# Optimization experiments

Measured on AMD Instinct MI355X. Metric: run time of the kernel, lower is better.

The kernel has to match this reference:

```python
import jax, jax.numpy as jnp
import numpy as np

N_NODES = 100000
N_EDGES = 1600000
HIDDEN = 128
N_STRUCT = 6
N_LAYERS = 3
BN_EPS = 1e-5


def setup_inputs() -> dict:
    key = jax.random.key(0)
    ks = jax.random.split(key, 8)
    edge_index = jax.random.randint(ks[0], (2, N_EDGES), 0, N_NODES, dtype=jnp.int32)
    struct_feats = jax.random.uniform(ks[1], (N_NODES, N_STRUCT), dtype=jnp.float32)
    emb_weight = jax.random.normal(ks[2], (N_NODES, HIDDEN - N_STRUCT), dtype=jnp.float32) * 0.1
    proj_w = jax.random.normal(ks[3], (N_STRUCT, N_STRUCT), dtype=jnp.float32) * 0.4
    proj_b = jnp.zeros((N_STRUCT,), jnp.float32)
    conv_w = jax.random.normal(ks[4], (N_LAYERS, HIDDEN, HIDDEN), dtype=jnp.float32) * (1.0 / np.sqrt(HIDDEN))
    conv_b = jnp.zeros((N_LAYERS, HIDDEN), jnp.float32)
    bn_gamma = jnp.ones((N_LAYERS, HIDDEN), jnp.float32)
    bn_beta = jnp.zeros((N_LAYERS, HIDDEN), jnp.float32)
    bn_mean = jnp.zeros((N_LAYERS, HIDDEN), jnp.float32)
    bn_var = jnp.ones((N_LAYERS, HIDDEN), jnp.float32)
    return {
        'edge_index': edge_index, 'struct_feats': struct_feats,
        'emb_weight': emb_weight, 'proj_w': proj_w, 'proj_b': proj_b,
        'conv_w': conv_w, 'conv_b': conv_b,
        'bn_gamma': bn_gamma, 'bn_beta': bn_beta,
        'bn_mean': bn_mean, 'bn_var': bn_var,
    }


def _encode(edge_index, struct_feats, emb_weight, proj_w, proj_b,
            conv_w, conv_b, bn_gamma, bn_beta, bn_mean, bn_var):
    src, dst = edge_index[0], edge_index[1]
    # GCN symmetric normalization (no self loops): deg over destination index
    deg = jax.ops.segment_sum(jnp.ones_like(src, dtype=jnp.float32), dst,
                              num_segments=N_NODES)
    dinv = jnp.where(deg > 0, jax.lax.rsqrt(deg), 0.0)
    norm = dinv[src] * dinv[dst]  # [E]

    # node features: learned embedding || projected structural features
    sf = jax.nn.relu(struct_feats @ proj_w + proj_b)
    x = jnp.concatenate([emb_weight, sf], axis=1)  # [N, HIDDEN]

    for i in range(N_LAYERS):
        x_prev = x
        h = x @ conv_w[i]  # [N, H]
        msg = h[src] * norm[:, None]  # gather + scale, [E, H]
        agg = jax.ops.segment_sum(msg, dst, num_segments=N_NODES) + conv_b[i]
        # BatchNorm1d (eval mode, running stats)
        x = (agg - bn_mean[i]) * (bn_gamma[i] * jax.lax.rsqrt(bn_var[i] + BN_EPS)) + bn_beta[i]
        x = jax.nn.relu(x)
        if i > 0:
            x = x + 0.5 * x_prev
    return x


def reference(edge_index, struct_feats, emb_weight, proj_w, proj_b,
              conv_w, conv_b, bn_gamma, bn_beta, bn_mean, bn_var):
    return _encode(edge_index, struct_feats, emb_weight, proj_w, proj_b,
                   conv_w, conv_b, bn_gamma, bn_beta, bn_mean, bn_var)
```

## Files before the change

### kernel.cpp

```cpp
#include <hip/hip_runtime.h>
#include <hip/hip_fp16.h>

#define N_NODES 100000
#define N_EDGES 1600000
#define HIDDEN  128
#define EMB_DIM 122
#define NSTRUCT 6
#define BN_EPS  1e-5f

__global__ void k_count_deg(const int* __restrict__ dst, int* __restrict__ deg,
                            int* __restrict__ rank) {
    int i = blockIdx.x * blockDim.x + threadIdx.x;
    if (i < N_EDGES) rank[i] = atomicAdd(&deg[dst[i]], 1);
}

#define SCAN_B 256
__global__ void k_scan1(const int* __restrict__ deg, int* __restrict__ bsum) {
    __shared__ int s[SCAN_B];
    int t = threadIdx.x;
    int i = blockIdx.x * SCAN_B + t;
    s[t] = (i < N_NODES) ? deg[i] : 0;
    __syncthreads();
    for (int off = SCAN_B / 2; off > 0; off >>= 1) {
        if (t < off) s[t] += s[t + off];
        __syncthreads();
    }
    if (t == 0) bsum[blockIdx.x] = s[0];
}

__global__ void k_scan2(int* __restrict__ bsum, int nb, int* __restrict__ ptrN) {
    __shared__ int s[512];
    int t = threadIdx.x;
    int v = (t < nb) ? bsum[t] : 0;
    s[t] = v;
    __syncthreads();
    for (int off = 1; off < 512; off <<= 1) {
        int u = (t >= off) ? s[t - off] : 0;
        __syncthreads();
        s[t] += u;
        __syncthreads();
    }
    if (t < nb) bsum[t] = s[t] - v;
    if (t == nb - 1) *ptrN = s[t];
}

__global__ void k_scan3(const int* __restrict__ deg, const int* __restrict__ bsum,
                        int* __restrict__ ptr) {
    __shared__ int s[SCAN_B];
    int t = threadIdx.x;
    int i = blockIdx.x * SCAN_B + t;
    int v = (i < N_NODES) ? deg[i] : 0;
    s[t] = v;
    __syncthreads();
    for (int off = 1; off < SCAN_B; off <<= 1) {
        int u = (t >= off) ? s[t - off] : 0;
        __syncthreads();
        s[t] += u;
        __syncthreads();
    }
    if (i < N_NODES) ptr[i] = bsum[blockIdx.x] + s[t] - v;
}

__global__ void k_fill(const int* __restrict__ src, const int* __restrict__ dst,
                       const int* __restrict__ rank,
                       const int* __restrict__ deg, const int* __restrict__ ptr,
                       int2* __restrict__ edges) {
    int i = blockIdx.x * blockDim.x + threadIdx.x;
    if (i < N_EDGES) {
        int s = src[i], d = dst[i];
        int ds = deg[s], dd = deg[d];
        float ns = (ds > 0) ? rsqrtf((float)ds) : 0.0f;
        float nd = (dd > 0) ? rsqrtf((float)dd) : 0.0f;
        int pos = ptr[d] + rank[i];
        edges[pos] = make_int2(s, __float_as_int(ns * nd));
    }
}

__global__ void k_node_init(const float* __restrict__ emb, const float* __restrict__ sfeat,
                            const float* __restrict__ pw, const float* __restrict__ pb,
                            float* __restrict__ x) {
    int idx = blockIdx.x * blockDim.x + threadIdx.x;
    if (idx >= N_NODES * HIDDEN) return;
    int n = idx >> 7, c = idx & 127;
    float v;
    if (c < EMB_DIM) {
        v = emb[n * EMB_DIM + c];
    } else {
        int j = c - EMB_DIM;
        float a = pb[j];
        #pragma unroll
        for (int k = 0; k < NSTRUCT; ++k) a += sfeat[n * NSTRUCT + k] * pw[k * NSTRUCT + j];
        v = fmaxf(a, 0.0f);
    }
    x[idx] = v;
}

__global__ __launch_bounds__(256, 3)
void k_gemm(const float* __restrict__ x, const float* __restrict__ W,
            __half* __restrict__ h) {
    __shared__ float Ws[64 * HIDDEN];
    __shared__ float xs[64][65];

    const int tid = threadIdx.x;
    const int n0  = blockIdx.x * 64;
    const int cg  = tid & 15;
    const int rg  = tid >> 4;
    const int c0  = cg * 4;
    const int r0  = rg * 4;

    float acc[4][8];
    #pragma unroll
    for (int i = 0; i < 4; ++i)
        #pragma unroll
        for (int j = 0; j < 8; ++j) acc[i][j] = 0.0f;

    for (int kk = 0; kk < HIDDEN; kk += 64) {
        for (int i = tid; i < 64 * HIDDEN; i += 256) Ws[i] = W[kk * HIDDEN + i];
        for (int i = tid; i < 64 * 64; i += 256) {
            int r = i >> 6, k = i & 63;
            int gn = n0 + r;
            xs[r][k] = (gn < N_NODES) ? x[(size_t)gn * HIDDEN + kk + k] : 0.0f;
        }
        __syncthreads();

        #pragma unroll 4
        for (int k = 0; k < 64; ++k) {
            float4 wa = *reinterpret_cast<const float4*>(&Ws[k * HIDDEN + c0]);
            float4 wb = *reinterpret_cast<const float4*>(&Ws[k * HIDDEN + c0 + 64]);
            #pragma unroll
            for (int i = 0; i < 4; ++i) {
                float xv = xs[r0 + i][k];
                acc[i][0] = fmaf(xv, wa.x, acc[i][0]);
                acc[i][1] = fmaf(xv, wa.y, acc[i][1]);
                acc[i][2] = fmaf(xv, wa.z, acc[i][2]);
                acc[i][3] = fmaf(xv, wa.w, acc[i][3]);
                acc[i][4] = fmaf(xv, wb.x, acc[i][4]);
                acc[i][5] = fmaf(xv, wb.y, acc[i][5]);
                acc[i][6] = fmaf(xv, wb.z, acc[i][6]);
                acc[i][7] = fmaf(xv, wb.w, acc[i][7]);
            }
        }
        __syncthreads();
    }

    #pragma unroll
    for (int i = 0; i < 4; ++i) {
        int gn = n0 + r0 + i;
        if (gn < N_NODES) {
            union { uint2 u; __half2 h2[2]; } p0, p1;
            p0.h2[0] = __floats2half2_rn(acc[i][0], acc[i][1]);
            p0.h2[1] = __floats2half2_rn(acc[i][2], acc[i][3]);
            p1.h2[0] = __floats2half2_rn(acc[i][4], acc[i][5]);
            p1.h2[1] = __floats2half2_rn(acc[i][6], acc[i][7]);
            *reinterpret_cast<uint2*>(&h[(size_t)gn * HIDDEN + c0])      = p0.u;
            *reinterpret_cast<uint2*>(&h[(size_t)gn * HIDDEN + c0 + 64]) = p1.u;
        }
    }
}

__global__ __launch_bounds__(256)
void k_agg(const __half* __restrict__ h, const int* __restrict__ ptr,
           const int2* __restrict__ edges,
           const float* __restrict__ bias, const float* __restrict__ mean,
           const float* __restrict__ var, const float* __restrict__ gamma,
           const float* __restrict__ beta,
           const float* __restrict__ xprev, int has_resid,
           float* __restrict__ out) {
    int node = blockIdx.x * 4 + (threadIdx.x >> 6);
    if (node >= N_NODES) return;
    const int lane = threadIdx.x & 63;
    const int q    = lane >> 4;
    const int sl   = lane & 15;
    const int c0   = sl * 8;
    int s = ptr[node], e = ptr[node + 1];

    float acc[8];
    #pragma unroll
    for (int k = 0; k < 8; ++k) acc[k] = 0.0f;

    for (int j0 = s; j0 < e; j0 += 64) {
        int nb  = min(64, e - j0);
        int idx = j0 + lane;
        int2 rec = (idx < e) ? edges[idx] : make_int2(0, 0);
        #pragma unroll 2
        for (int jj = 0; jj < nb; jj += 4) {
            int   sv = __shfl(rec.x, jj + q);
            float nv = __int_as_float(__shfl(rec.y, jj + q));
            union { uint4 u; __half2 h2[4]; } v;
            v.u = *reinterpret_cast<const uint4*>(h + ((size_t)sv << 7) + c0);
            #pragma unroll
            for (int k = 0; k < 4; ++k) {
                float2 f = __half22float2(v.h2[k]);
                acc[2 * k]     = fmaf(nv, f.x, acc[2 * k]);
                acc[2 * k + 1] = fmaf(nv, f.y, acc[2 * k + 1]);
            }
        }
    }

    #pragma unroll
    for (int k = 0; k < 8; ++k) {
        acc[k] += __shfl_xor(acc[k], 16);
        acc[k] += __shfl_xor(acc[k], 32);
    }

    if (q == 0) {
        float4 bi0 = *reinterpret_cast<const float4*>(bias  + c0);
        float4 bi1 = *reinterpret_cast<const float4*>(bias  + c0 + 4);
        float4 mu0 = *reinterpret_cast<const float4*>(mean  + c0);
        float4 mu1 = *reinterpret_cast<const float4*>(mean  + c0 + 4);
        float4 va0 = *reinterpret_cast<const float4*>(var   + c0);
        float4 va1 = *reinterpret_cast<const float4*>(var   + c0 + 4);
        float4 ga0 = *reinterpret_cast<const float4*>(gamma + c0);
        float4 ga1 = *reinterpret_cast<const float4*>(gamma + c0 + 4);
        float4 be0 = *reinterpret_cast<const float4*>(beta  + c0);
        float4 be1 = *reinterpret_cast<const float4*>(beta  + c0 + 4);
        float4 y0, y1;
        y0.x = fmaxf((acc[0] + bi0.x - mu0.x) * (ga0.x * rsqrtf(va0.x + BN_EPS)) + be0.x, 0.0f);
        y0.y = fmaxf((acc[1] + bi0.y - mu0.y) * (ga0.y * rsqrtf(va0.y + BN_EPS)) + be0.y, 0.0f);
        y0.z = fmaxf((acc[2] + bi0.z - mu0.z) * (ga0.z * rsqrtf(va0.z + BN_EPS)) + be0.z, 0.0f);
        y0.w = fmaxf((acc[3] + bi0.w - mu0.w) * (ga0.w * rsqrtf(va0.w + BN_EPS)) + be0.w, 0.0f);
        y1.x = fmaxf((acc[4] + bi1.x - mu1.x) * (ga1.x * rsqrtf(va1.x + BN_EPS)) + be1.x, 0.0f);
        y1.y = fmaxf((acc[5] + bi1.y - mu1.y) * (ga1.y * rsqrtf(va1.y + BN_EPS)) + be1.y, 0.0f);
        y1.z = fmaxf((acc[6] + bi1.z - mu1.z) * (ga1.z * rsqrtf(va1.z + BN_EPS)) + be1.z, 0.0f);
        y1.w = fmaxf((acc[7] + bi1.w - mu1.w) * (ga1.w * rsqrtf(va1.w + BN_EPS)) + be1.w, 0.0f);
        size_t o = ((size_t)node << 7) + c0;
        if (has_resid) {
            float4 xp0 = *reinterpret_cast<const float4*>(xprev + o);
            float4 xp1 = *reinterpret_cast<const float4*>(xprev + o + 4);
            y0.x += 0.5f * xp0.x;  y0.y += 0.5f * xp0.y;
            y0.z += 0.5f * xp0.z;  y0.w += 0.5f * xp0.w;
            y1.x += 0.5f * xp1.x;  y1.y += 0.5f * xp1.y;
            y1.z += 0.5f * xp1.z;  y1.w += 0.5f * xp1.w;
        }
        *reinterpret_cast<float4*>(out + o)     = y0;
        *reinterpret_cast<float4*>(out + o + 4) = y1;
    }
}

extern "C" void kernel_launch(void* const* d_in, const int* in_sizes, int n_in,
                              void* d_out, int out_size, void* d_ws, size_t ws_size,
                              hipStream_t stream) {
    const int*   ei    = (const int*)d_in[0];
    const int*   src   = ei;
    const int*   dst   = ei + N_EDGES;
    const float* sfeat = (const float*)d_in[1];
    const float* emb   = (const float*)d_in[2];
    const float* pw    = (const float*)d_in[3];
    const float* pb    = (const float*)d_in[4];
    const float* convw = (const float*)d_in[5];
    const float* convb = (const float*)d_in[6];
    const float* gamma = (const float*)d_in[7];
    const float* beta  = (const float*)d_in[8];
    const float* mean  = (const float*)d_in[9];
    const float* var   = (const float*)d_in[10];
    float* out = (float*)d_out;

    char* wsc = (char*)d_ws;
    auto alloc = [&](size_t bytes) -> void* {
        void* p = (void*)wsc;
        wsc += (bytes + 255) & ~(size_t)255;
        return p;
    };
    int*    deg   = (int*)   alloc(N_NODES * sizeof(int));
    int*    rank  = (int*)   alloc((size_t)N_EDGES * sizeof(int));
    int*    ptr   = (int*)   alloc((N_NODES + 1) * sizeof(int));
    int*    bsum  = (int*)   alloc(512 * sizeof(int));
    int2*   edges = (int2*)  alloc((size_t)N_EDGES * sizeof(int2));
    float*  bufA  = (float*) alloc((size_t)N_NODES * HIDDEN * sizeof(float));
    __half* hbuf  = (__half*)alloc((size_t)N_NODES * HIDDEN * sizeof(__half));

    const int nb = (N_NODES + SCAN_B - 1) / SCAN_B;

    hipMemsetAsync(deg, 0, N_NODES * sizeof(int), stream);

    k_count_deg<<<N_EDGES / 256, 256, 0, stream>>>(dst, deg, rank);
    k_scan1<<<nb, SCAN_B, 0, stream>>>(deg, bsum);
    k_scan2<<<1, 512, 0, stream>>>(bsum, nb, &ptr[N_NODES]);
    k_scan3<<<nb, SCAN_B, 0, stream>>>(deg, bsum, ptr);
    k_fill<<<N_EDGES / 256, 256, 0, stream>>>(src, dst, rank, deg, ptr, edges);
    k_node_init<<<(N_NODES * HIDDEN) / 256, 256, 0, stream>>>(emb, sfeat, pw, pb, bufA);

    const int ggrid = (N_NODES + 63) / 64;
    const int agrid = (N_NODES + 3) / 4;

    k_gemm<<<ggrid, 256, 0, stream>>>(bufA, convw + 0 * HIDDEN * HIDDEN, hbuf);
    k_agg<<<agrid, 256, 0, stream>>>(hbuf, ptr, edges,
                                     convb + 0 * HIDDEN, mean + 0 * HIDDEN, var + 0 * HIDDEN,
                                     gamma + 0 * HIDDEN, beta + 0 * HIDDEN,
                                     nullptr, 0, bufA);
    k_gemm<<<ggrid, 256, 0, stream>>>(bufA, convw + 1 * HIDDEN * HIDDEN, hbuf);
    k_agg<<<agrid, 256, 0, stream>>>(hbuf, ptr, edges,
                                     convb + 1 * HIDDEN, mean + 1 * HIDDEN, var + 1 * HIDDEN,
                                     gamma + 1 * HIDDEN, beta + 1 * HIDDEN,
                                     bufA, 1, out);
    k_gemm<<<ggrid, 256, 0, stream>>>(out, convw + 2 * HIDDEN * HIDDEN, hbuf);
    k_agg<<<agrid, 256, 0, stream>>>(hbuf, ptr, edges,
                                     convb + 2 * HIDDEN, mean + 2 * HIDDEN, var + 2 * HIDDEN,
                                     gamma + 2 * HIDDEN, beta + 2 * HIDDEN,
                                     out, 1, out);
    (void)in_sizes; (void)n_in; (void)out_size; (void)ws_size;
}
```

Baseline: 667.1 us.

## Use fp16 MFMA for per-layer GEMM with pre-transposed half weights

Replaces the FP32 shared-memory tiled GEMM with a wave-level MFMA 16x16x32 f16 kernel. Activations are converted to fp16 in registers and weights are read from a transposed fp16 copy, which a new small kernel produces once per call. The aim is to cut the compute cost of the dense transform. In exchange, GEMM inputs now carry fp16 rounding, and the output stores are scattered 2-byte writes rather than vectorized ones.

```diff
diff --git a/kernel.cpp b/kernel.cpp
--- a/kernel.cpp
+++ b/kernel.cpp
@@ -7,6 +7,9 @@
 #define EMB_DIM 122
 #define NSTRUCT 6
 #define BN_EPS  1e-5f
+
+typedef _Float16 f16x8 __attribute__((ext_vector_type(8)));
+typedef float    f32x4 __attribute__((ext_vector_type(4)));
 
 __global__ void k_count_deg(const int* __restrict__ dst, int* __restrict__ deg,
                             int* __restrict__ rank) {
@@ -95,65 +98,59 @@
     x[idx] = v;
 }
 
-__global__ __launch_bounds__(256, 3)
-void k_gemm(const float* __restrict__ x, const float* __restrict__ W,
+__global__ void k_wcvt(const float* __restrict__ W, __half* __restrict__ Wt) {
+    int idx = blockIdx.x * blockDim.x + threadIdx.x;
+    int l = idx >> 14, rem = idx & 16383, n = rem >> 7, k = rem & 127;
+    Wt[idx] = __float2half(W[l * 16384 + k * 128 + n]);
+}
+
+__global__ __launch_bounds__(256)
+void k_gemm(const float* __restrict__ x, const __half* __restrict__ Wt,
             __half* __restrict__ h) {
-    __shared__ float Ws[64 * HIDDEN];
-    __shared__ float xs[64][65];
-
-    const int tid = threadIdx.x;
-    const int n0  = blockIdx.x * 64;
-    const int cg  = tid & 15;
-    const int rg  = tid >> 4;
-    const int c0  = cg * 4;
-    const int r0  = rg * 4;
-
-    float acc[4][8];
-    #pragma unroll
-    for (int i = 0; i < 4; ++i)
+    const int tid  = threadIdx.x;
+    const int w    = tid >> 6;
+    const int lane = tid & 63;
+    const int g    = lane >> 4;
+    const int m15  = lane & 15;
+
+    const int rowA = blockIdx.x * 64 + w * 16 + m15;
+    const bool rok = (rowA < N_NODES);
+
+    f32x4 acc[8];
+    #pragma unroll
+    for (int nt = 0; nt < 8; ++nt) acc[nt] = (f32x4){0.f, 0.f, 0.f, 0.f};
+
+    #pragma unroll
+    for (int kc = 0; kc < 4; ++kc) {
+        const int k0 = kc * 32 + g * 8;
+        f16x8 a;
+        if (rok) {
+            const float4 p0 = *reinterpret_cast<const float4*>(x + (size_t)rowA * HIDDEN + k0);
+            const float4 p1 = *reinterpret_cast<const float4*>(x + (size_t)rowA * HIDDEN + k0 + 4);
+            a[0] = (_Float16)p0.x; a[1] = (_Float16)p0.y;
+            a[2] = (_Float16)p0.z; a[3] = (_Float16)p0.w;
+            a[4] = (_Float16)p1.x; a[5] = (_Float16)p1.y;
+            a[6] = (_Float16)p1.z; a[7] = (_Float16)p1.w;
+        } else {
+            a = (f16x8)(_Float16)0;
+        }
         #pragma unroll
-        for (int j = 0; j < 8; ++j) acc[i][j] = 0.0f;
-
-    for (int kk = 0; kk < HIDDEN; kk += 64) {
-        for (int i = tid; i < 64 * HIDDEN; i += 256) Ws[i] = W[kk * HIDDEN + i];
-        for (int i = tid; i < 64 * 64; i += 256) {
-            int r = i >> 6, k = i & 63;
-            int gn = n0 + r;
-            xs[r][k] = (gn < N_NODES) ? x[(size_t)gn * HIDDEN + kk + k] : 0.0f;
-        }
-        __syncthreads();
-
-        #pragma unroll 4
-        for (int k = 0; k < 64; ++k) {
-            float4 wa = *reinterpret_cast<const float4*>(&Ws[k * HIDDEN + c0]);
-            float4 wb = *reinterpret_cast<const float4*>(&Ws[k * HIDDEN + c0 + 64]);
-            #pragma unroll
-            for (int i = 0; i < 4; ++i) {
-                float xv = xs[r0 + i][k];
-                acc[i][0] = fmaf(xv, wa.x, acc[i][0]);
-                acc[i][1] = fmaf(xv, wa.y, acc[i][1]);
-                acc[i][2] = fmaf(xv, wa.z, acc[i][2]);
-                acc[i][3] = fmaf(xv, wa.w, acc[i][3]);
-                acc[i][4] = fmaf(xv, wb.x, acc[i][4]);
-                acc[i][5] = fmaf(xv, wb.y, acc[i][5]);
-                acc[i][6] = fmaf(xv, wb.z, acc[i][6]);
-                acc[i][7] = fmaf(xv, wb.w, acc[i][7]);
-            }
-        }
-        __syncthreads();
-    }
-
-    #pragma unroll
-    for (int i = 0; i < 4; ++i) {
-        int gn = n0 + r0 + i;
-        if (gn < N_NODES) {
-            union { uint2 u; __half2 h2[2]; } p0, p1;
-            p0.h2[0] = __floats2half2_rn(acc[i][0], acc[i][1]);
-            p0.h2[1] = __floats2half2_rn(acc[i][2], acc[i][3]);
-            p1.h2[0] = __floats2half2_rn(acc[i][4], acc[i][5]);
-            p1.h2[1] = __floats2half2_rn(acc[i][6], acc[i][7]);
-            *reinterpret_cast<uint2*>(&h[(size_t)gn * HIDDEN + c0])      = p0.u;
-            *reinterpret_cast<uint2*>(&h[(size_t)gn * HIDDEN + c0 + 64]) = p1.u;
+        for (int nt = 0; nt < 8; ++nt) {
+            const int n = nt * 16 + m15;
+            f16x8 b = *reinterpret_cast<const f16x8*>(Wt + (size_t)n * HIDDEN + k0);
+            acc[nt] = __builtin_amdgcn_mfma_f32_16x16x32_f16(a, b, acc[nt], 0, 0, 0);
+        }
+    }
+
+    const int growbase = blockIdx.x * 64 + w * 16 + g * 4;
+    #pragma unroll
+    for (int nt = 0; nt < 8; ++nt) {
+        const int col = nt * 16 + m15;
+        #pragma unroll
+        for (int r = 0; r < 4; ++r) {
+            const int grow = growbase + r;
+            if (grow < N_NODES)
+                h[(size_t)grow * HIDDEN + col] = __float2half(acc[nt][r]);
         }
     }
 }
@@ -268,12 +265,14 @@
     int2*   edges = (int2*)  alloc((size_t)N_EDGES * sizeof(int2));
     float*  bufA  = (float*) alloc((size_t)N_NODES * HIDDEN * sizeof(float));
     __half* hbuf  = (__half*)alloc((size_t)N_NODES * HIDDEN * sizeof(__half));
+    __half* wt    = (__half*)alloc(3 * HIDDEN * HIDDEN * sizeof(__half));
 
     const int nb = (N_NODES + SCAN_B - 1) / SCAN_B;
 
     hipMemsetAsync(deg, 0, N_NODES * sizeof(int), stream);
 
     k_count_deg<<<N_EDGES / 256, 256, 0, stream>>>(dst, deg, rank);
+    k_wcvt<<<(3 * HIDDEN * HIDDEN) / 256, 256, 0, stream>>>(convw, wt);
     k_scan1<<<nb, SCAN_B, 0, stream>>>(deg, bsum);
     k_scan2<<<1, 512, 0, stream>>>(bsum, nb, &ptr[N_NODES]);
     k_scan3<<<nb, SCAN_B, 0, stream>>>(deg, bsum, ptr);
@@ -283,17 +282,17 @@
     const int ggrid = (N_NODES + 63) / 64;
     const int agrid = (N_NODES + 3) / 4;
 
-    k_gemm<<<ggrid, 256, 0, stream>>>(bufA, convw + 0 * HIDDEN * HIDDEN, hbuf);
+    k_gemm<<<ggrid, 256, 0, stream>>>(bufA, wt + 0 * HIDDEN * HIDDEN, hbuf);
     k_agg<<<agrid, 256, 0, stream>>>(hbuf, ptr, edges,
                                      convb + 0 * HIDDEN, mean + 0 * HIDDEN, var + 0 * HIDDEN,
                                      gamma + 0 * HIDDEN, beta + 0 * HIDDEN,
                                      nullptr, 0, bufA);
-    k_gemm<<<ggrid, 256, 0, stream>>>(bufA, convw + 1 * HIDDEN * HIDDEN, hbuf);
+    k_gemm<<<ggrid, 256, 0, stream>>>(bufA, wt + 1 * HIDDEN * HIDDEN, hbuf);
     k_agg<<<agrid, 256, 0, stream>>>(hbuf, ptr, edges,
                                      convb + 1 * HIDDEN, mean + 1 * HIDDEN, var + 1 * HIDDEN,
                                      gamma + 1 * HIDDEN, beta + 1 * HIDDEN,
                                      bufA, 1, out);
-    k_gemm<<<ggrid, 256, 0, stream>>>(out, convw + 2 * HIDDEN * HIDDEN, hbuf);
+    k_gemm<<<ggrid, 256, 0, stream>>>(out, wt + 2 * HIDDEN * HIDDEN, hbuf);
     k_agg<<<agrid, 256, 0, stream>>>(hbuf, ptr, edges,
                                      convb + 2 * HIDDEN, mean + 2 * HIDDEN, var + 2 * HIDDEN,
                                      gamma + 2 * HIDDEN, beta + 2 * HIDDEN,
```

After: 608.3 us. -8.8%, faster.
